# Kernel optimization log

Measured on AMD Instinct MI355X. Metric: run time of the kernel, lower is better.

The kernel has to match this reference:

```python
import jax, jax.numpy as jnp
import numpy as np

B, N, ND = 32, 512, 8        # batch, graph_size, node_dim
L, H, D = 4, 8, 512          # layers, heads, embed_dim
DK = D // H                  # key_dim = val_dim = 64
F = 2048                     # feed_forward_hidden
EPS = 1e-5


def setup_inputs() -> dict:
    key = jax.random.key(0)
    ks = jax.random.split(key, 16)
    u = lambda k, shape, s: jax.random.uniform(k, shape, jnp.float32, -s, s)
    x = jax.random.normal(ks[0], (B, N, ND), dtype=jnp.float32)
    mask = jax.random.randint(ks[1], (B, N, N), 0, 2).astype(jnp.int32)  # 1 = masked
    return {
        "x": x,
        "mask": mask,
        # init_embed Linear(node_dim, embed_dim)
        "We": u(ks[2], (ND, D), 1.0 / np.sqrt(ND)),
        "be": u(ks[3], (D,), 1.0 / np.sqrt(ND)),
        # per-head projections, stacked over layers; torch init: uniform(-1/sqrt(last_dim), ...)
        "Wq": u(ks[4], (L, H, D, DK), 1.0 / np.sqrt(DK)),
        "Wk": u(ks[5], (L, H, D, DK), 1.0 / np.sqrt(DK)),
        "Wv": u(ks[6], (L, H, D, DK), 1.0 / np.sqrt(DK)),
        "Wo": u(ks[7], (L, H, DK, D), 1.0 / np.sqrt(D)),
        # BatchNorm1d affine params (torch default: weight=1, bias=0)
        "g1": jnp.ones((L, D), jnp.float32), "bt1": jnp.zeros((L, D), jnp.float32),
        "g2": jnp.ones((L, D), jnp.float32), "bt2": jnp.zeros((L, D), jnp.float32),
        # FFN
        "W1": u(ks[8], (L, D, F), 1.0 / np.sqrt(D)),
        "bf1": u(ks[9], (L, F), 1.0 / np.sqrt(D)),
        "W2": u(ks[10], (L, F, D), 1.0 / np.sqrt(F)),
        "bf2": u(ks[11], (L, D), 1.0 / np.sqrt(F)),
    }


def _batch_norm(h, g, b):
    # BatchNorm1d in training mode over flattened (B*N, D), biased variance
    hf = h.reshape(-1, h.shape[-1])
    mu = hf.mean(axis=0)
    var = hf.var(axis=0)
    return (h - mu) * jax.lax.rsqrt(var + EPS) * g + b


def reference(x, mask, We, be, Wq, Wk, Wv, Wo, g1, bt1, W1, bf1, W2, bf2, g2, bt2):
    m = mask.astype(bool)[None]                      # [1,B,N,N], True = masked
    scale = 1.0 / np.sqrt(Wq.shape[-1])
    h = x @ We + be                                  # [B,N,D]
    for l in range(Wq.shape[0]):
        # hand-rolled per-head MHA (q = h, self-attention)
        Q = jnp.einsum('bnd,hdk->hbnk', h, Wq[l])
        K = jnp.einsum('bnd,hdk->hbnk', h, Wk[l])
        V = jnp.einsum('bnd,hdv->hbnv', h, Wv[l])
        scores = jnp.einsum('hbqk,hbnk->hbqn', Q, K) * scale   # [H,B,N,N]
        scores = jnp.where(m, -jnp.inf, scores)
        attn = jax.nn.softmax(scores, axis=-1)
        attn = jnp.where(m, 0.0, attn)               # second mask-zeroing pass
        heads = jnp.einsum('hbqn,hbnv->hbqv', attn, V)
        out = jnp.einsum('hbqv,hvd->bqd', heads, Wo[l])
        h = _batch_norm(h + out, g1[l], bt1[l])      # residual + BN
        ff = jax.nn.relu(h @ W1[l] + bf1[l]) @ W2[l] + bf2[l]
        h = _batch_norm(h + ff, g2[l], bt2[l])       # residual + BN
    return (h, h.mean(axis=1))
```

## Files before the change

### kernel.cpp

```cpp
#include <hip/hip_runtime.h>
#include <hip/hip_fp16.h>
#include <math.h>

#define BN_ROWS 16384
#define DIM 512
#define FF 2048
#define LAYERS 4
#define NSEQ 512
#define BATCH 32

typedef _Float16 f16;
typedef __attribute__((ext_vector_type(8))) _Float16 f16x8;
typedef __attribute__((ext_vector_type(4))) _Float16 f16x4;
typedef __attribute__((ext_vector_type(4))) float f32x4;
typedef unsigned long long u64;

__device__ __forceinline__ f32x4 mfma_f16(f16x8 a, f16x8 b, f32x4 c) {
    return __builtin_amdgcn_mfma_f32_16x16x32_f16(a, b, c, 0, 0, 0);
}
__device__ __forceinline__ void gload_lds16(const f16* g, f16* l) {
    __builtin_amdgcn_global_load_lds(
        (const __attribute__((address_space(1))) unsigned int*)g,
        (__attribute__((address_space(3))) unsigned int*)l, 16, 0, 0);
}

__global__ __launch_bounds__(256)
void pack_qkv(const float* __restrict__ Wq, const float* __restrict__ Wk,
              const float* __restrict__ Wv, f16* __restrict__ oh) {
    size_t i = (size_t)blockIdx.x * 256 + threadIdx.x;
    int d = i & 511;
    size_t rr = i >> 9;
    int row = (int)(rr % 1536);
    int lay = (int)(rr / 1536);
    int which = row >> 9, hh = (row >> 6) & 7, k = row & 63;
    const float* W = which == 0 ? Wq : which == 1 ? Wk : Wv;
    oh[i] = (f16)W[(((size_t)lay * 8 + hh) * 512 + d) * 64 + k];
}

__global__ __launch_bounds__(256)
void transpose_w(const float* __restrict__ in, f16* __restrict__ oh, int R, int C) {
    size_t i = (size_t)blockIdx.x * 256 + threadIdx.x;
    int r = (int)(i % R);
    size_t t = i / R;
    int c = (int)(t % C);
    int lay = (int)(t / C);
    oh[i] = (f16)in[((size_t)lay * R + r) * C + c];
}

__global__ __launch_bounds__(256)
void pack_mask(const int* __restrict__ mask, u64* __restrict__ pm) {
    int wid = (blockIdx.x * 256 + threadIdx.x) >> 6;
    int lane = threadIdx.x & 63;
    for (int i = 0; i < 64; i++) {
        size_t word = (size_t)wid * 64 + i;
        u64 bal = __ballot(mask[word * 64 + lane] != 0);
        if (lane == 0) pm[word] = bal;
    }
}

__global__ __launch_bounds__(512)
void embed_kernel(const float* __restrict__ x, const float* __restrict__ We,
                  const float* __restrict__ be, float* __restrict__ h,
                  f16* __restrict__ hf) {
    int row = blockIdx.x, d = threadIdx.x;
    const float* xr = x + (size_t)row * 8;
    float acc = be[d];
#pragma unroll
    for (int c = 0; c < 8; c++) acc += xr[c] * We[c * DIM + d];
    size_t idx = (size_t)row * DIM + d;
    h[idx] = acc;
    hf[idx] = (f16)acc;
}

template<int OUT>
__global__ __launch_bounds__(256)
void gemm_f16(const f16* __restrict__ A, const f16* __restrict__ Bt,
              const float* __restrict__ bias,
              void* __restrict__ O0, void* __restrict__ O1, void* __restrict__ O2,
              int M, int N, int K) {
    __shared__ f16 As[2][4096];
    __shared__ f16 Bs[2][4096];
    const int gx = gridDim.x;
    const int nwg = gx * gridDim.y;
    const int id = blockIdx.y * gx + blockIdx.x;
    const int chunk = nwg >> 3;
    const int sid = (id & 7) * chunk + (id >> 3);
    const int row0 = (sid / gx) * 128, col0 = (sid % gx) * 128;

    const int tid = threadIdx.x, l = tid & 63, w = tid >> 6;
    const int wr = w >> 1, wc = w & 1;
    const int fr = l & 15, fq = l >> 4;
    const int srow = l >> 2, skg = (l & 3) * 8;

    f32x4 acc[4][4] = {};
    const f16* Ab = A + (size_t)(row0 + w * 32 + srow) * K + skg;
    const f16* Bb = Bt + (size_t)(col0 + w * 32 + srow) * K + skg;
    const size_t a16 = (size_t)16 * K;
    const int nt = K >> 5;

    gload_lds16(Ab,       &As[0][(w * 2 + 0) * 512]);
    gload_lds16(Ab + a16, &As[0][(w * 2 + 1) * 512]);
    gload_lds16(Bb,       &Bs[0][(w * 2 + 0) * 512]);
    gload_lds16(Bb + a16, &Bs[0][(w * 2 + 1) * 512]);

    for (int kt = 0; kt < nt; kt++) {
        const int buf = kt & 1;
        __syncthreads();
        if (kt + 1 < nt) {
            const int k0 = (kt + 1) * 32;
            gload_lds16(Ab + k0,       &As[buf ^ 1][(w * 2 + 0) * 512]);
            gload_lds16(Ab + a16 + k0, &As[buf ^ 1][(w * 2 + 1) * 512]);
            gload_lds16(Bb + k0,       &Bs[buf ^ 1][(w * 2 + 0) * 512]);
            gload_lds16(Bb + a16 + k0, &Bs[buf ^ 1][(w * 2 + 1) * 512]);
        }
        f16x8 a[4], b[4];
#pragma unroll
        for (int i = 0; i < 4; i++)
            a[i] = *(const f16x8*)&As[buf][(wr * 64 + i * 16 + fr) * 32 + fq * 8];
#pragma unroll
        for (int j = 0; j < 4; j++)
            b[j] = *(const f16x8*)&Bs[buf][(wc * 64 + j * 16 + fr) * 32 + fq * 8];
#pragma unroll
        for (int i = 0; i < 4; i++)
#pragma unroll
            for (int j = 0; j < 4; j++)
                acc[i][j] = mfma_f16(a[i], b[j], acc[i][j]);
    }

    if (OUT == 1) {
        f16* C = (f16*)O0;
#pragma unroll
        for (int j = 0; j < 4; j++) {
            int gcol = col0 + wc * 64 + j * 16 + fr;
            float bv = bias[gcol];
#pragma unroll
            for (int i = 0; i < 4; i++) {
                int gr = row0 + wr * 64 + i * 16 + fq * 4;
#pragma unroll
                for (int r = 0; r < 4; r++)
                    C[(size_t)(gr + r) * N + gcol] = (f16)fmaxf(acc[i][j][r] + bv, 0.f);
            }
        }
    } else if (OUT == 2) {
        f16* Qo = (f16*)O0; f16* Ko = (f16*)O1; f16* Vo = (f16*)O2;
#pragma unroll
        for (int j = 0; j < 4; j++) {
            int gcol = col0 + wc * 64 + j * 16 + fr;
            if (gcol < 1024) {
                f16* dst = gcol < 512 ? Qo : Ko;
                int cc = gcol & 511;
#pragma unroll
                for (int i = 0; i < 4; i++) {
                    int gr = row0 + wr * 64 + i * 16 + fq * 4;
#pragma unroll
                    for (int r = 0; r < 4; r++)
                        dst[(size_t)(gr + r) * 512 + cc] = (f16)acc[i][j][r];
                }
            } else {
                int hh = (gcol - 1024) >> 6, v = gcol & 63;
#pragma unroll
                for (int i = 0; i < 4; i++) {
                    int gr = row0 + wr * 64 + i * 16 + fq * 4;
                    int b = gr >> 9, n = gr & 511;
                    f16x4 sv;
#pragma unroll
                    for (int r = 0; r < 4; r++) sv[r] = (f16)acc[i][j][r];
                    *(f16x4*)&Vo[(((size_t)b * 8 + hh) * 64 + v) * 512 + n] = sv;
                }
            }
        }
    } else {
        float* hres = (float*)O0;
        float* st   = (float*)O1;
#pragma unroll
        for (int j = 0; j < 4; j++) {
            int gcol = col0 + wc * 64 + j * 16 + fr;
            float bv = bias ? bias[gcol] : 0.f;
            float csum = 0.f, csq = 0.f;
#pragma unroll
            for (int i = 0; i < 4; i++) {
                int gr = row0 + wr * 64 + i * 16 + fq * 4;
#pragma unroll
                for (int r = 0; r < 4; r++) {
                    size_t idx = (size_t)(gr + r) * N + gcol;
                    float v = acc[i][j][r] + bv + hres[idx];
                    hres[idx] = v;
                    csum += v; csq += v * v;
                }
            }
            csum += __shfl_down(csum, 32, 64); csum += __shfl_down(csum, 16, 64);
            csq  += __shfl_down(csq,  32, 64); csq  += __shfl_down(csq,  16, 64);
            if (fq == 0) {
                atomicAdd(&st[gcol], csum);
                atomicAdd(&st[gcol + 512], csq);
            }
        }
    }
}

__global__ __launch_bounds__(256)
void attn_flash(const f16* __restrict__ Q, const f16* __restrict__ Kg,
                const f16* __restrict__ Vt, const u64* __restrict__ pmask,
                f16* __restrict__ attf) {
    int id = blockIdx.x;
    int wgid = (id & 7) * 128 + (id >> 3);
    int qc = wgid & 3;
    int gid = wgid >> 2;
    int b = gid & 31, hd = gid >> 5;

    __shared__ f16 Kl[2][4096];
    __shared__ f16 Vl[2][4096];
    __shared__ f16 Plds[4][1024];

    const int tid = threadIdx.x, w = tid >> 6, l = tid & 63;
    const int fr = l & 15, fq = l >> 4;

    const int brow = qc * 128 + w * 32;
    const size_t qbase = ((size_t)b * NSEQ + brow) * DIM + hd * 64;
    f16x8 qa[2][2];
#pragma unroll
    for (int sub = 0; sub < 2; sub++)
#pragma unroll
        for (int ks = 0; ks < 2; ks++)
            qa[sub][ks] = *(const f16x8*)(Q + qbase + (size_t)(sub * 16 + fr) * DIM + ks * 32 + fq * 8);

    const f16* ksrc = Kg + (size_t)b * NSEQ * DIM + hd * 64;
    const f16* vsrc = Vt + ((size_t)b * 8 + hd) * 64 * 512;
    const u64* mrow = pmask + ((size_t)b * NSEQ + brow) * 8;

    const int sr = tid & 63;
    const int sg0 = tid >> 6;
    const int sg1 = sg0 + 4;

    const float SC = 0.18033688011112042f;
    const float THR = 11.0f;

    float mu[2][4];
    f32x4 O[2][4] = {};
    f32x4 S1[2] = {};
#pragma unroll
    for (int s = 0; s < 2; s++)
#pragma unroll
        for (int r = 0; r < 4; r++) mu[s][r] = -1e30f;

    f16x8 vones;
#pragma unroll
    for (int i = 0; i < 8; i++) vones[i] = (f16)1.0f;

    char* Pb = (char*)&Plds[w][0];

    gload_lds16(ksrc + (size_t)sr * DIM + sg0 * 8, &Kl[0][tid * 8]);
    gload_lds16(ksrc + (size_t)sr * DIM + sg1 * 8, &Kl[0][2048 + tid * 8]);
    gload_lds16(vsrc + (size_t)sr * 512 + sg0 * 8, &Vl[0][tid * 8]);
    gload_lds16(vsrc + (size_t)sr * 512 + sg1 * 8, &Vl[0][2048 + tid * 8]);

    for (int c = 0; c < 8; c++) {
        const int buf = c & 1;
        __syncthreads();
        if (c < 7) {
            const int n1 = (c + 1) * 64;
            gload_lds16(ksrc + (size_t)(n1 + sr) * DIM + sg0 * 8, &Kl[buf ^ 1][tid * 8]);
            gload_lds16(ksrc + (size_t)(n1 + sr) * DIM + sg1 * 8, &Kl[buf ^ 1][2048 + tid * 8]);
            gload_lds16(vsrc + (size_t)sr * 512 + n1 + sg0 * 8,   &Vl[buf ^ 1][tid * 8]);
            gload_lds16(vsrc + (size_t)sr * 512 + n1 + sg1 * 8,   &Vl[buf ^ 1][2048 + tid * 8]);
        }

        f16x8 kb[4][2];
#pragma unroll
        for (int nt = 0; nt < 4; nt++)
#pragma unroll
            for (int ks = 0; ks < 2; ks++)
                kb[nt][ks] = *(const f16x8*)&Kl[buf][(ks * 4 + fq) * 512 + (nt * 16 + fr) * 8];

        f32x4 ps[2][4];
#pragma unroll
        for (int sub = 0; sub < 2; sub++)
#pragma unroll
            for (int nt = 0; nt < 4; nt++) {
                f32x4 a = {};
                a = mfma_f16(qa[sub][0], kb[nt][0], a);
                a = mfma_f16(qa[sub][1], kb[nt][1], a);
                ps[sub][nt] = a;
            }
#pragma unroll
        for (int sub = 0; sub < 2; sub++)
#pragma unroll
            for (int rr = 0; rr < 4; rr++) {
                u64 bits = mrow[(size_t)(sub * 16 + fq * 4 + rr) * 8 + c];
#pragma unroll
                for (int nt = 0; nt < 4; nt++) {
                    float u = ps[sub][nt][rr] * SC;
                    ps[sub][nt][rr] = ((bits >> (nt * 16 + fr)) & 1ull) ? -INFINITY : u;
                }
            }

        f16x8 vb[4][2];
#pragma unroll
        for (int vt = 0; vt < 4; vt++)
#pragma unroll
            for (int ks = 0; ks < 2; ks++)
                vb[vt][ks] = *(const f16x8*)&Vl[buf][(ks * 4 + fq) * 512 + (vt * 16 + fr) * 8];

#pragma unroll
        for (int sub = 0; sub < 2; sub++) {
            float lmax[4];
#pragma unroll
            for (int rr = 0; rr < 4; rr++)
                lmax[rr] = fmaxf(fmaxf(ps[sub][0][rr], ps[sub][1][rr]),
                                 fmaxf(ps[sub][2][rr], ps[sub][3][rr]));
            bool over = (lmax[0] > mu[sub][0] + THR) | (lmax[1] > mu[sub][1] + THR) |
                        (lmax[2] > mu[sub][2] + THR) | (lmax[3] > mu[sub][3] + THR);
            if (__any(over)) {
#pragma unroll
                for (int rr = 0; rr < 4; rr++) {
                    float v = lmax[rr];
#pragma unroll
                    for (int msk = 1; msk < 16; msk <<= 1)
                        v = fmaxf(v, __shfl_xor(v, msk, 64));
                    float mn = fmaxf(mu[sub][rr], v);
                    float sc = exp2f(mu[sub][rr] - mn);
                    mu[sub][rr] = mn;
                    S1[sub][rr] *= sc;
#pragma unroll
                    for (int vt = 0; vt < 4; vt++)
                        O[sub][vt][rr] *= sc;
                }
            }
#pragma unroll
            for (int nt = 0; nt < 4; nt++)
#pragma unroll
                for (int rr = 0; rr < 4; rr++)
                    ps[sub][nt][rr] = exp2f(ps[sub][nt][rr] - mu[sub][rr]);
#pragma unroll
            for (int nt = 0; nt < 4; nt++)
#pragma unroll
                for (int rr = 0; rr < 4; rr++) {
                    int row = fq * 4 + rr;
                    int byte = ((row * 64 + nt * 16 + fr) * 2) ^ ((row & 7) << 4);
                    *(f16*)(Pb + byte) = (f16)ps[sub][nt][rr];
                }
            f16x8 pa[2];
#pragma unroll
            for (int ks = 0; ks < 2; ks++) {
                int byte = ((fr * 64 + ks * 32 + fq * 8) * 2) ^ ((fr & 7) << 4);
                pa[ks] = *(const f16x8*)(Pb + byte);
            }
            S1[sub] = mfma_f16(pa[0], vones, S1[sub]);
            S1[sub] = mfma_f16(pa[1], vones, S1[sub]);
#pragma unroll
            for (int vt = 0; vt < 4; vt++) {
                O[sub][vt] = mfma_f16(pa[0], vb[vt][0], O[sub][vt]);
                O[sub][vt] = mfma_f16(pa[1], vb[vt][1], O[sub][vt]);
            }
        }
    }
#pragma unroll
    for (int sub = 0; sub < 2; sub++) {
        float inv[4];
#pragma unroll
        for (int rr = 0; rr < 4; rr++) inv[rr] = 1.f / S1[sub][rr];
#pragma unroll
        for (int vt = 0; vt < 4; vt++)
#pragma unroll
            for (int rr = 0; rr < 4; rr++) {
                float v = O[sub][vt][rr] * inv[rr];
                size_t idx = ((size_t)b * NSEQ + brow + sub * 16 + fq * 4 + rr) * DIM
                             + hd * 64 + vt * 16 + fr;
                attf[idx] = (f16)v;
            }
    }
}

__global__ __launch_bounds__(256)
void bn_apply(float* __restrict__ h, f16* __restrict__ hf,
              const float* __restrict__ sums, const float* __restrict__ g,
              const float* __restrict__ bt, float* __restrict__ outp) {
    size_t i4 = (size_t)blockIdx.x * 256 + threadIdx.x;
    size_t idx = i4 * 4;
    int c = (int)(idx & (DIM - 1));
    float4 hv = *(float4*)&h[idx];
    float4 s4 = *(const float4*)&sums[c];
    float4 q4 = *(const float4*)&sums[DIM + c];
    float4 g4 = *(const float4*)&g[c];
    float4 b4 = *(const float4*)&bt[c];
    float o[4];
    const float invn = 1.f / BN_ROWS;
#pragma unroll
    for (int j = 0; j < 4; j++) {
        float mu = ((const float*)&s4)[j] * invn;
        float var = ((const float*)&q4)[j] * invn - mu * mu;
        o[j] = (((const float*)&hv)[j] - mu) * rsqrtf(var + 1e-5f)
               * ((const float*)&g4)[j] + ((const float*)&b4)[j];
    }
    *(float4*)&h[idx] = *(float4*)o;
    if (outp) *(float4*)&outp[idx] = *(float4*)o;
    f16x4 s;
#pragma unroll
    for (int j = 0; j < 4; j++) s[j] = (f16)o[j];
    *(f16x4*)&hf[idx] = s;
}

__global__ __launch_bounds__(512)
void mean_kernel(const float* __restrict__ src, float* __restrict__ out2) {
    int b = blockIdx.x, seg = blockIdx.y, d = threadIdx.x;
    float acc = 0.f;
    for (int n = seg * 64; n < seg * 64 + 64; n++)
        acc += src[((size_t)b * NSEQ + n) * DIM + d];
    atomicAdd(&out2[b * DIM + d], acc * (1.f / NSEQ));
}

extern "C" void kernel_launch(void* const* d_in, const int* in_sizes, int n_in,
                              void* d_out, int out_size, void* d_ws, size_t ws_size,
                              hipStream_t stream) {
    const float* x   = (const float*)d_in[0];
    const int*   mask= (const int*)d_in[1];
    const float* We  = (const float*)d_in[2];
    const float* be  = (const float*)d_in[3];
    const float* Wq  = (const float*)d_in[4];
    const float* Wk  = (const float*)d_in[5];
    const float* Wv  = (const float*)d_in[6];
    const float* Wo  = (const float*)d_in[7];
    const float* g1  = (const float*)d_in[8];
    const float* bt1 = (const float*)d_in[9];
    const float* g2  = (const float*)d_in[10];
    const float* bt2 = (const float*)d_in[11];
    const float* W1  = (const float*)d_in[12];
    const float* bf1 = (const float*)d_in[13];
    const float* W2  = (const float*)d_in[14];
    const float* bf2 = (const float*)d_in[15];
    float* out = (float*)d_out;

    const size_t MiB = 1ull << 20;
    const size_t M1 = (size_t)BN_ROWS * DIM;
    char* base = (char*)d_ws;
    float* h     = (float*)base;
    f16*   hf    = (f16*)(base + 32 * MiB);
    f16*   Qf    = (f16*)(base + 48 * MiB);
    f16*   Kf    = (f16*)(base + 64 * MiB);
    f16*   Vt    = (f16*)(base + 80 * MiB);
    f16*   attf  = (f16*)(base + 96 * MiB);
    f16*   ffh   = (f16*)(base + 48 * MiB);
    float* stats = (float*)(base + 112 * MiB);
    u64*   pmask = (u64*)(base + 112 * MiB + 65536);
    f16*   wqkv  = (f16*)(base + 114 * MiB);
    f16*   wo    = wqkv + (size_t)4 * 1536 * 512;
    f16*   w1t   = wo   + (size_t)4 * 512 * 512;
    f16*   w2t   = w1t  + (size_t)4 * 2048 * 512;

    pack_qkv<<<dim3(4 * 1536 * 512 / 256), dim3(256), 0, stream>>>(Wq, Wk, Wv, wqkv);
    transpose_w<<<dim3(4 * 512 * 512 / 256), dim3(256), 0, stream>>>(Wo, wo, 512, 512);
    transpose_w<<<dim3(4 * 512 * 2048 / 256), dim3(256), 0, stream>>>(W1, w1t, 512, 2048);
    transpose_w<<<dim3(4 * 2048 * 512 / 256), dim3(256), 0, stream>>>(W2, w2t, 2048, 512);
    pack_mask<<<dim3(512), dim3(256), 0, stream>>>(mask, pmask);
    hipMemsetAsync(out + M1, 0, BATCH * DIM * sizeof(float), stream);

    embed_kernel<<<dim3(BN_ROWS), dim3(512), 0, stream>>>(x, We, be, h, hf);

    for (int l = 0; l < LAYERS; l++) {
        gemm_f16<2><<<dim3(1536 / 128, 128), dim3(256), 0, stream>>>(
            hf, wqkv + (size_t)l * 1536 * 512, nullptr, Qf, Kf, Vt,
            BN_ROWS, 1536, 512);

        attn_flash<<<dim3(1024), dim3(256), 0, stream>>>(Qf, Kf, Vt, pmask, attf);

        hipMemsetAsync(stats, 0, 1024 * sizeof(float), stream);
        gemm_f16<3><<<dim3(512 / 128, 128), dim3(256), 0, stream>>>(
            attf, wo + (size_t)l * 512 * 512, nullptr, h, stats, nullptr,
            BN_ROWS, 512, 512);
        bn_apply<<<dim3(M1 / 1024), dim3(256), 0, stream>>>(
            h, hf, stats, g1 + l * DIM, bt1 + l * DIM, nullptr);

        hipMemsetAsync(stats, 0, 1024 * sizeof(float), stream);
        gemm_f16<1><<<dim3(FF / 128, BN_ROWS / 128), dim3(256), 0, stream>>>(
            hf, w1t + (size_t)l * FF * DIM, bf1 + (size_t)l * FF,
            ffh, nullptr, nullptr, BN_ROWS, FF, DIM);
        gemm_f16<3><<<dim3(DIM / 128, BN_ROWS / 128), dim3(256), 0, stream>>>(
            ffh, w2t + (size_t)l * DIM * FF, bf2 + (size_t)l * DIM,
            h, stats, nullptr, BN_ROWS, DIM, FF);

        float* outp = (l == LAYERS - 1) ? out : nullptr;
        bn_apply<<<dim3(M1 / 1024), dim3(256), 0, stream>>>(
            h, hf, stats, g2 + l * DIM, bt2 + l * DIM, outp);
    }

    mean_kernel<<<dim3(BATCH, 8), dim3(512), 0, stream>>>(out, out + M1);
}
```

Measured before the change: 1.224 ms.

## Add 128x64 GEMM tile for N=512 GEMMs, fold softmax scale into Q, set MFMA priority

Templates the GEMM on the N tile width and uses a 128x64 tile for the Wo and W2 projections, where N is only 512. This doubles the workgroup count from 512 to 1024 so more of the CUs are busy, at the cost of less B-tile reuse per block. It also moves the softmax scale into the Q store of the QKV GEMM epilogue, which removes a per-element multiply inside attention. Finally it raises wave priority with s_setprio around the MFMA blocks in attention. Rounding Q to f16 after scaling changes precision slightly.

```diff
diff --git a/kernel.cpp b/kernel.cpp
--- a/kernel.cpp
+++ b/kernel.cpp
@@ -72,95 +72,110 @@
     hf[idx] = (f16)acc;
 }
 
-template<int OUT>
+template<int OUT, int BN>
 __global__ __launch_bounds__(256)
 void gemm_f16(const f16* __restrict__ A, const f16* __restrict__ Bt,
               const float* __restrict__ bias,
               void* __restrict__ O0, void* __restrict__ O1, void* __restrict__ O2,
               int M, int N, int K) {
+    constexpr int NI = (BN == 128) ? 4 : 2;
     __shared__ f16 As[2][4096];
-    __shared__ f16 Bs[2][4096];
+    __shared__ f16 Bs[2][BN * 32];
     const int gx = gridDim.x;
     const int nwg = gx * gridDim.y;
     const int id = blockIdx.y * gx + blockIdx.x;
     const int chunk = nwg >> 3;
     const int sid = (id & 7) * chunk + (id >> 3);
-    const int row0 = (sid / gx) * 128, col0 = (sid % gx) * 128;
+    const int row0 = (sid / gx) * 128, col0 = (sid % gx) * BN;
 
     const int tid = threadIdx.x, l = tid & 63, w = tid >> 6;
     const int wr = w >> 1, wc = w & 1;
     const int fr = l & 15, fq = l >> 4;
     const int srow = l >> 2, skg = (l & 3) * 8;
 
-    f32x4 acc[4][4] = {};
+    f32x4 acc[NI][4] = {};
     const f16* Ab = A + (size_t)(row0 + w * 32 + srow) * K + skg;
-    const f16* Bb = Bt + (size_t)(col0 + w * 32 + srow) * K + skg;
+    const f16* Bb = (BN == 128)
+        ? Bt + (size_t)(col0 + w * 32 + srow) * K + skg
+        : Bt + (size_t)(col0 + w * 16 + srow) * K + skg;
     const size_t a16 = (size_t)16 * K;
     const int nt = K >> 5;
 
-    gload_lds16(Ab,       &As[0][(w * 2 + 0) * 512]);
-    gload_lds16(Ab + a16, &As[0][(w * 2 + 1) * 512]);
-    gload_lds16(Bb,       &Bs[0][(w * 2 + 0) * 512]);
-    gload_lds16(Bb + a16, &Bs[0][(w * 2 + 1) * 512]);
+    auto stage = [&](int buf, int k0) {
+        gload_lds16(Ab + k0,       &As[buf][(w * 2 + 0) * 512]);
+        gload_lds16(Ab + a16 + k0, &As[buf][(w * 2 + 1) * 512]);
+        if (BN == 128) {
+            gload_lds16(Bb + k0,       &Bs[buf][(w * 2 + 0) * 512]);
+            gload_lds16(Bb + a16 + k0, &Bs[buf][(w * 2 + 1) * 512]);
+        } else {
+            gload_lds16(Bb + k0,       &Bs[buf][w * 512]);
+        }
+    };
+
+    stage(0, 0);
 
     for (int kt = 0; kt < nt; kt++) {
         const int buf = kt & 1;
         __syncthreads();
-        if (kt + 1 < nt) {
-            const int k0 = (kt + 1) * 32;
-            gload_lds16(Ab + k0,       &As[buf ^ 1][(w * 2 + 0) * 512]);
-            gload_lds16(Ab + a16 + k0, &As[buf ^ 1][(w * 2 + 1) * 512]);
-            gload_lds16(Bb + k0,       &Bs[buf ^ 1][(w * 2 + 0) * 512]);
-            gload_lds16(Bb + a16 + k0, &Bs[buf ^ 1][(w * 2 + 1) * 512]);
-        }
-        f16x8 a[4], b[4];
-#pragma unroll
-        for (int i = 0; i < 4; i++)
-            a[i] = *(const f16x8*)&As[buf][(wr * 64 + i * 16 + fr) * 32 + fq * 8];
-#pragma unroll
-        for (int j = 0; j < 4; j++)
-            b[j] = *(const f16x8*)&Bs[buf][(wc * 64 + j * 16 + fr) * 32 + fq * 8];
-#pragma unroll
-        for (int i = 0; i < 4; i++)
+        if (kt + 1 < nt) stage(buf ^ 1, (kt + 1) * 32);
+        f16x8 a[NI], b[4];
+#pragma unroll
+        for (int i = 0; i < NI; i++) {
+            int rb = (BN == 128) ? wr * 64 + i * 16 : w * 32 + i * 16;
+            a[i] = *(const f16x8*)&As[buf][(rb + fr) * 32 + fq * 8];
+        }
+#pragma unroll
+        for (int j = 0; j < 4; j++) {
+            int cb = (BN == 128) ? wc * 64 + j * 16 : j * 16;
+            b[j] = *(const f16x8*)&Bs[buf][(cb + fr) * 32 + fq * 8];
+        }
+#pragma unroll
+        for (int i = 0; i < NI; i++)
 #pragma unroll
             for (int j = 0; j < 4; j++)
                 acc[i][j] = mfma_f16(a[i], b[j], acc[i][j]);
     }
 
+    const int rowb = (BN == 128) ? wr * 64 : w * 32;
+    const int colb = (BN == 128) ? wc * 64 : 0;
+
     if (OUT == 1) {
         f16* C = (f16*)O0;
 #pragma unroll
         for (int j = 0; j < 4; j++) {
-            int gcol = col0 + wc * 64 + j * 16 + fr;
+            int gcol = col0 + colb + j * 16 + fr;
             float bv = bias[gcol];
 #pragma unroll
-            for (int i = 0; i < 4; i++) {
-                int gr = row0 + wr * 64 + i * 16 + fq * 4;
+            for (int i = 0; i < NI; i++) {
+                int gr = row0 + rowb + i * 16 + fq * 4;
 #pragma unroll
                 for (int r = 0; r < 4; r++)
                     C[(size_t)(gr + r) * N + gcol] = (f16)fmaxf(acc[i][j][r] + bv, 0.f);
             }
         }
     } else if (OUT == 2) {
+        const float SCQ = 0.18033688011112042f;
         f16* Qo = (f16*)O0; f16* Ko = (f16*)O1; f16* Vo = (f16*)O2;
 #pragma unroll
         for (int j = 0; j < 4; j++) {
-            int gcol = col0 + wc * 64 + j * 16 + fr;
+            int gcol = col0 + colb + j * 16 + fr;
             if (gcol < 1024) {
-                f16* dst = gcol < 512 ? Qo : Ko;
+                bool isQ = gcol < 512;
+                f16* dst = isQ ? Qo : Ko;
+                float sc = isQ ? SCQ : 1.0f;
                 int cc = gcol & 511;
 #pragma unroll
-                for (int i = 0; i < 4; i++) {
-                    int gr = row0 + wr * 64 + i * 16 + fq * 4;
+                for (int i = 0; i < NI; i++) {
+                    int gr = row0 + rowb + i * 16 + fq * 4;
 #pragma unroll
                     for (int r = 0; r < 4; r++)
-                        dst[(size_t)(gr + r) * 512 + cc] = (f16)acc[i][j][r];
+                        dst[(size_t)(gr + r) * 512 + cc] = (f16)(acc[i][j][r] * sc);
                 }
             } else {
                 int hh = (gcol - 1024) >> 6, v = gcol & 63;
 #pragma unroll
-                for (int i = 0; i < 4; i++) {
-                    int gr = row0 + wr * 64 + i * 16 + fq * 4;
+                for (int i = 0; i < NI; i++) {
+                    int gr = row0 + rowb + i * 16 + fq * 4;
                     int b = gr >> 9, n = gr & 511;
                     f16x4 sv;
 #pragma unroll
@@ -174,12 +189,12 @@
         float* st   = (float*)O1;
 #pragma unroll
         for (int j = 0; j < 4; j++) {
-            int gcol = col0 + wc * 64 + j * 16 + fr;
+            int gcol = col0 + colb + j * 16 + fr;
             float bv = bias ? bias[gcol] : 0.f;
             float csum = 0.f, csq = 0.f;
 #pragma unroll
-            for (int i = 0; i < 4; i++) {
-                int gr = row0 + wr * 64 + i * 16 + fq * 4;
+            for (int i = 0; i < NI; i++) {
+                int gr = row0 + rowb + i * 16 + fq * 4;
 #pragma unroll
                 for (int r = 0; r < 4; r++) {
                     size_t idx = (size_t)(gr + r) * N + gcol;
@@ -232,7 +247,6 @@
     const int sg0 = tid >> 6;
     const int sg1 = sg0 + 4;
 
-    const float SC = 0.18033688011112042f;
     const float THR = 11.0f;
 
     float mu[2][4];
@@ -273,6 +287,7 @@
                 kb[nt][ks] = *(const f16x8*)&Kl[buf][(ks * 4 + fq) * 512 + (nt * 16 + fr) * 8];
 
         f32x4 ps[2][4];
+        __builtin_amdgcn_s_setprio(1);
 #pragma unroll
         for (int sub = 0; sub < 2; sub++)
 #pragma unroll
@@ -282,16 +297,15 @@
                 a = mfma_f16(qa[sub][1], kb[nt][1], a);
                 ps[sub][nt] = a;
             }
+        __builtin_amdgcn_s_setprio(0);
 #pragma unroll
         for (int sub = 0; sub < 2; sub++)
 #pragma unroll
             for (int rr = 0; rr < 4; rr++) {
                 u64 bits = mrow[(size_t)(sub * 16 + fq * 4 + rr) * 8 + c];
 #pragma unroll
-                for (int nt = 0; nt < 4; nt++) {
-                    float u = ps[sub][nt][rr] * SC;
-                    ps[sub][nt][rr] = ((bits >> (nt * 16 + fr)) & 1ull) ? -INFINITY : u;
-                }
+                for (int nt = 0; nt < 4; nt++)
+                    if ((bits >> (nt * 16 + fr)) & 1ull) ps[sub][nt][rr] = -INFINITY;
             }
 
         f16x8 vb[4][2];
@@ -345,6 +359,7 @@
                 int byte = ((fr * 64 + ks * 32 + fq * 8) * 2) ^ ((fr & 7) << 4);
                 pa[ks] = *(const f16x8*)(Pb + byte);
             }
+            __builtin_amdgcn_s_setprio(1);
             S1[sub] = mfma_f16(pa[0], vones, S1[sub]);
             S1[sub] = mfma_f16(pa[1], vones, S1[sub]);
 #pragma unroll
@@ -352,6 +367,7 @@
                 O[sub][vt] = mfma_f16(pa[0], vb[vt][0], O[sub][vt]);
                 O[sub][vt] = mfma_f16(pa[1], vb[vt][1], O[sub][vt]);
             }
+            __builtin_amdgcn_s_setprio(0);
         }
     }
 #pragma unroll
@@ -457,24 +473,24 @@
     embed_kernel<<<dim3(BN_ROWS), dim3(512), 0, stream>>>(x, We, be, h, hf);
 
     for (int l = 0; l < LAYERS; l++) {
-        gemm_f16<2><<<dim3(1536 / 128, 128), dim3(256), 0, stream>>>(
+        gemm_f16<2, 128><<<dim3(1536 / 128, 128), dim3(256), 0, stream>>>(
             hf, wqkv + (size_t)l * 1536 * 512, nullptr, Qf, Kf, Vt,
             BN_ROWS, 1536, 512);
 
         attn_flash<<<dim3(1024), dim3(256), 0, stream>>>(Qf, Kf, Vt, pmask, attf);
 
         hipMemsetAsync(stats, 0, 1024 * sizeof(float), stream);
-        gemm_f16<3><<<dim3(512 / 128, 128), dim3(256), 0, stream>>>(
+        gemm_f16<3, 64><<<dim3(512 / 64, 128), dim3(256), 0, stream>>>(
             attf, wo + (size_t)l * 512 * 512, nullptr, h, stats, nullptr,
             BN_ROWS, 512, 512);
         bn_apply<<<dim3(M1 / 1024), dim3(256), 0, stream>>>(
             h, hf, stats, g1 + l * DIM, bt1 + l * DIM, nullptr);
 
         hipMemsetAsync(stats, 0, 1024 * sizeof(float), stream);
-        gemm_f16<1><<<dim3(FF / 128, BN_ROWS / 128), dim3(256), 0, stream>>>(
+        gemm_f16<1, 128><<<dim3(FF / 128, BN_ROWS / 128), dim3(256), 0, stream>>>(
             hf, w1t + (size_t)l * FF * DIM, bf1 + (size_t)l * FF,
             ffh, nullptr, nullptr, BN_ROWS, FF, DIM);
-        gemm_f16<3><<<dim3(DIM / 128, BN_ROWS / 128), dim3(256), 0, stream>>>(
+        gemm_f16<3, 64><<<dim3(512 / 64, 128), dim3(256), 0, stream>>>(
             ffh, w2t + (size_t)l * DIM * FF, bf2 + (size_t)l * DIM,
             h, stats, nullptr, BN_ROWS, DIM, FF);
 
```

After: 1.267 ms. 1.04x slower.
